# Kernel optimization log

Measured on AMD Instinct MI355X. Metric: run time of the kernel, lower is better.

Reference implementation:

```python
import jax, jax.numpy as jnp
import numpy as np

N_HEAD = 16

def setup_inputs() -> dict:
    key = jax.random.key(0)
    ks = jax.random.split(key, 9)
    B, T, C = 1, 4096, 1024
    s = 1.0 / np.sqrt(C)
    x = jax.random.normal(ks[0], (B, T, C), dtype=jnp.float32)
    Wq = jax.random.uniform(ks[1], (C, C), jnp.float32, -s, s)
    bq = jax.random.uniform(ks[2], (C,), jnp.float32, -s, s)
    Wk = jax.random.uniform(ks[3], (C, C), jnp.float32, -s, s)
    bk = jax.random.uniform(ks[4], (C,), jnp.float32, -s, s)
    Wv = jax.random.uniform(ks[5], (C, C), jnp.float32, -s, s)
    bv = jax.random.uniform(ks[6], (C,), jnp.float32, -s, s)
    Wp = jax.random.uniform(ks[7], (C, C), jnp.float32, -s, s)
    bp = jax.random.uniform(ks[8], (C,), jnp.float32, -s, s)
    return {"x": x, "Wq": Wq, "bq": bq, "Wk": Wk, "bk": bk,
            "Wv": Wv, "bv": bv, "Wp": Wp, "bp": bp}

def reference(x, Wq, bq, Wk, bk, Wv, bv, Wp, bp):
    B, T, C = x.shape
    H = N_HEAD
    D = C // H
    # projections -> (B, H, T, D)
    def proj(W, b):
        return (x @ W.T + b).reshape(B, T, H, D).transpose(0, 2, 1, 3)
    q, k, v = proj(Wq, bq), proj(Wk, bk), proj(Wv, bv)
    scale = 1.0 / np.sqrt(D).astype(np.float32)
    att = jnp.einsum('bhtd,bhsd->bhts', q, k) * scale  # (B,H,T,T)
    causal = jnp.tril(jnp.ones((T, T), dtype=bool))
    att = jnp.where(causal[None, None], att, -jnp.inf)
    att = jax.nn.softmax(att, axis=-1)
    y = jnp.einsum('bhts,bhsd->bhtd', att, v)  # (B,H,T,D)
    y = y.transpose(0, 2, 1, 3).reshape(B, T, C)
    return y @ Wp.T + bp
```

## Files before the change

### kernel.cpp

```cpp
#include <hip/hip_runtime.h>
#include <hip/hip_bf16.h>
#include <math.h>

typedef __bf16 bf16x8 __attribute__((ext_vector_type(8)));
typedef __bf16 bf16x4 __attribute__((ext_vector_type(4)));
typedef float f32x4 __attribute__((ext_vector_type(4)));

#define MFMA_BF16 __builtin_amdgcn_mfma_f32_16x16x32_bf16

#define QSCALE 0.18033688011112042f

__device__ inline void async_load16(const __hip_bfloat16* g, __hip_bfloat16* l) {
    __builtin_amdgcn_global_load_lds(
        (const __attribute__((address_space(1))) unsigned int*)g,
        (__attribute__((address_space(3))) unsigned int*)l,
        16, 0, 0);
}

__device__ inline int sig(int x) {
    return (x & ~12) | ((x & 4) << 1) | ((x & 8) >> 1);
}

__device__ inline unsigned int pack_bf16_trunc(float lo, float hi) {
    return __builtin_amdgcn_perm(__float_as_uint(hi), __float_as_uint(lo),
                                 0x07060302u);
}

__global__ __launch_bounds__(256) void f32_to_bf16(
    const float* __restrict__ in, __hip_bfloat16* __restrict__ out, int n)
{
    const int i = (blockIdx.x * 256 + threadIdx.x) * 8;
    if (i >= n) return;
    const float4 a = *(const float4*)(in + i);
    const float4 b = *(const float4*)(in + i + 4);
    __hip_bfloat16 tmp[8];
    tmp[0] = __float2bfloat16(a.x); tmp[1] = __float2bfloat16(a.y);
    tmp[2] = __float2bfloat16(a.z); tmp[3] = __float2bfloat16(a.w);
    tmp[4] = __float2bfloat16(b.x); tmp[5] = __float2bfloat16(b.y);
    tmp[6] = __float2bfloat16(b.z); tmp[7] = __float2bfloat16(b.w);
    *(bf16x8*)(out + i) = *(const bf16x8*)tmp;
}

__global__ __launch_bounds__(256) void f32_to_bf16_w4(
    const float* __restrict__ w0, const float* __restrict__ w1,
    const float* __restrict__ w2, const float* __restrict__ w3,
    __hip_bfloat16* __restrict__ o0, __hip_bfloat16* __restrict__ o1,
    __hip_bfloat16* __restrict__ o2, __hip_bfloat16* __restrict__ o3, int n)
{
    const int y = blockIdx.y;
    const float* in = y == 0 ? w0 : y == 1 ? w1 : y == 2 ? w2 : w3;
    __hip_bfloat16* out = y == 0 ? o0 : y == 1 ? o1 : y == 2 ? o2 : o3;
    const int i = (blockIdx.x * 256 + threadIdx.x) * 8;
    if (i >= n) return;
    const float4 a = *(const float4*)(in + i);
    const float4 b = *(const float4*)(in + i + 4);
    __hip_bfloat16 tmp[8];
    tmp[0] = __float2bfloat16(a.x); tmp[1] = __float2bfloat16(a.y);
    tmp[2] = __float2bfloat16(a.z); tmp[3] = __float2bfloat16(a.w);
    tmp[4] = __float2bfloat16(b.x); tmp[5] = __float2bfloat16(b.y);
    tmp[6] = __float2bfloat16(b.z); tmp[7] = __float2bfloat16(b.w);
    *(bf16x8*)(out + i) = *(const bf16x8*)tmp;
}

__global__ __launch_bounds__(256) void transpose_bf16(
    const __hip_bfloat16* __restrict__ in, __hip_bfloat16* __restrict__ out,
    int R, int Cc)
{
    __shared__ __align__(16) __hip_bfloat16 tile[64][72];
    const int r0 = blockIdx.x * 64, c0 = blockIdx.y * 64;
    const int tid = threadIdx.x;
    #pragma unroll
    for (int it = 0; it < 2; ++it) {
        const int c = tid + it * 256;
        const int row = c >> 3, col = (c & 7) * 8;
        *(bf16x8*)&tile[row][col] = *(const bf16x8*)(in + (size_t)(r0 + row) * Cc + c0 + col);
    }
    __syncthreads();
    #pragma unroll
    for (int it = 0; it < 2; ++it) {
        const int c = tid + it * 256;
        const int drow = c >> 3, scol = (c & 7) * 8;
        __hip_bfloat16 tmp[8];
        #pragma unroll
        for (int j = 0; j < 8; ++j) tmp[j] = tile[scol + j][drow];
        *(bf16x8*)(out + (size_t)(c0 + drow) * R + r0 + scol) = *(const bf16x8*)tmp;
    }
}

__global__ __launch_bounds__(256) void gemm_qkv(
    const __hip_bfloat16* __restrict__ A,
    const __hip_bfloat16* __restrict__ B,
    const float* __restrict__ bq, const float* __restrict__ bk, const float* __restrict__ bv,
    __hip_bfloat16* __restrict__ Qo, __hip_bfloat16* __restrict__ Ko,
    __hip_bfloat16* __restrict__ Vo,
    int M, int K)
{
    __shared__ __align__(16) __hip_bfloat16 As[128 * 64];
    __shared__ __align__(16) __hip_bfloat16 Bs[128 * 64];

    const int tid  = threadIdx.x;
    const int lane = tid & 63;
    const int wave = tid >> 6;
    const int l15  = lane & 15;
    const int quad = lane >> 4;
    const int m0 = blockIdx.x * 128;
    const int n0 = blockIdx.y * 128;
    const int wr = wave >> 1, wc = wave & 1;
    const int sel = n0 >> 10;

    f32x4 acc[4][4] = {};

    int srow[4], scol[4];
    #pragma unroll
    for (int i = 0; i < 4; ++i) {
        const int c = tid + 256 * i;
        srow[i] = c >> 3;
        scol[i] = ((c & 7) ^ (srow[i] & 7)) * 8;
    }

    for (int k0 = 0; k0 < K; k0 += 64) {
        __syncthreads();
        #pragma unroll
        for (int i = 0; i < 4; ++i) {
            async_load16(A + (size_t)(m0 + srow[i]) * K + k0 + scol[i],
                         As + (size_t)(tid + 256 * i) * 8);
            async_load16(B + (size_t)(n0 + srow[i]) * K + k0 + scol[i],
                         Bs + (size_t)(tid + 256 * i) * 8);
        }
        __syncthreads();

        #pragma unroll
        for (int kd = 0; kd < 2; ++kd) {
            bf16x8 af[4], bfr[4];
            #pragma unroll
            for (int mi = 0; mi < 4; ++mi) {
                const int row = wr * 64 + mi * 16 + l15;
                af[mi] = *(const bf16x8*)(
                    As + row * 64 + (((kd * 4 + quad) ^ (row & 7)) << 3));
            }
            #pragma unroll
            for (int ni = 0; ni < 4; ++ni) {
                const int row = wc * 64 + ni * 16 + l15;
                bfr[ni] = *(const bf16x8*)(
                    Bs + row * 64 + (((kd * 4 + quad) ^ (row & 7)) << 3));
            }
            #pragma unroll
            for (int mi = 0; mi < 4; ++mi)
                #pragma unroll
                for (int ni = 0; ni < 4; ++ni)
                    acc[mi][ni] = MFMA_BF16(af[mi], bfr[ni], acc[mi][ni], 0, 0, 0);
        }
    }

    __hip_bfloat16* dst = sel == 0 ? Qo : (sel == 1 ? Ko : Vo);
    const float* bptr   = sel == 0 ? bq : (sel == 1 ? bk : bv);
    const float sc      = sel == 0 ? QSCALE : 1.0f;

    #pragma unroll
    for (int ni = 0; ni < 4; ++ni) {
        const int cc = (n0 + wc * 64 + ni * 16 + l15) & 1023;
        const float bias = bptr[cc];
        #pragma unroll
        for (int mi = 0; mi < 4; ++mi) {
            const int row = m0 + wr * 64 + mi * 16 + quad * 4;
            #pragma unroll
            for (int r = 0; r < 4; ++r)
                dst[(size_t)(row + r) * 1024 + cc] =
                    __float2bfloat16((acc[mi][ni][r] + bias) * sc);
        }
    }
}

__global__ __launch_bounds__(256) void gemm_out_f32(
    const __hip_bfloat16* __restrict__ A,
    const __hip_bfloat16* __restrict__ B,
    const float* __restrict__ bias,
    float* __restrict__ Cf,
    int M, int N, int K)
{
    __shared__ __align__(16) __hip_bfloat16 As[64 * 64];
    __shared__ __align__(16) __hip_bfloat16 Bs[128 * 64];

    const int tid  = threadIdx.x;
    const int lane = tid & 63;
    const int wave = tid >> 6;
    const int l15  = lane & 15;
    const int quad = lane >> 4;
    const int m0 = blockIdx.x * 64;
    const int n0 = blockIdx.y * 128;
    const int wr = wave >> 1, wc = wave & 1;

    f32x4 acc[2][4] = {};

    int srow[4], scol[4];
    #pragma unroll
    for (int i = 0; i < 4; ++i) {
        const int c = tid + 256 * i;
        srow[i] = c >> 3;
        scol[i] = ((c & 7) ^ (srow[i] & 7)) * 8;
    }

    for (int k0 = 0; k0 < K; k0 += 64) {
        __syncthreads();
        #pragma unroll
        for (int i = 0; i < 2; ++i)
            async_load16(A + (size_t)(m0 + srow[i]) * K + k0 + scol[i],
                         As + (size_t)(tid + 256 * i) * 8);
        #pragma unroll
        for (int i = 0; i < 4; ++i)
            async_load16(B + (size_t)(n0 + srow[i]) * K + k0 + scol[i],
                         Bs + (size_t)(tid + 256 * i) * 8);
        __syncthreads();

        #pragma unroll
        for (int kd = 0; kd < 2; ++kd) {
            bf16x8 af[2], bfr[4];
            #pragma unroll
            for (int mi = 0; mi < 2; ++mi) {
                const int row = wr * 32 + mi * 16 + l15;
                af[mi] = *(const bf16x8*)(
                    As + row * 64 + (((kd * 4 + quad) ^ (row & 7)) << 3));
            }
            #pragma unroll
            for (int ni = 0; ni < 4; ++ni) {
                const int row = wc * 64 + ni * 16 + l15;
                bfr[ni] = *(const bf16x8*)(
                    Bs + row * 64 + (((kd * 4 + quad) ^ (row & 7)) << 3));
            }
            #pragma unroll
            for (int mi = 0; mi < 2; ++mi)
                #pragma unroll
                for (int ni = 0; ni < 4; ++ni)
                    acc[mi][ni] = MFMA_BF16(af[mi], bfr[ni], acc[mi][ni], 0, 0, 0);
        }
    }

    #pragma unroll
    for (int ni = 0; ni < 4; ++ni) {
        const int col = n0 + wc * 64 + ni * 16 + l15;
        const float bv = bias[col];
        #pragma unroll
        for (int mi = 0; mi < 2; ++mi) {
            const int row = m0 + wr * 32 + mi * 16 + quad * 4;
            #pragma unroll
            for (int r = 0; r < 4; ++r)
                Cf[(size_t)(row + r) * N + col] = acc[mi][ni][r] + bv;
        }
    }
}

__global__ __launch_bounds__(512, 4) void attn_causal(
    const __hip_bfloat16* __restrict__ Q,
    const __hip_bfloat16* __restrict__ K,
    const __hip_bfloat16* __restrict__ Vt,
    __hip_bfloat16* __restrict__ PoB,
    float* __restrict__ PlB,
    int T, int C)
{
    const int h  = blockIdx.y;
    const int bx = blockIdx.x;
    const int j  = bx & 7;
    const int sq = bx >> 3;
    const int tid  = threadIdx.x;
    const int w    = tid >> 6;
    const int lane = tid & 63;
    const int l15  = lane & 15;
    const int quad = lane >> 4;

    __hip_bfloat16* Po = PoB + (size_t)sq * T * C;
    float* Pl = PlB + (size_t)sq * (size_t)(T / 64) * 64 * 16;

    const int len1 = j + 1, len2 = 16 - j;
    const int tile1 = j,    tile2 = 15 - j;
    const int kb1 = len1 * sq, kb2 = len2 * sq;

    __shared__ __align__(16) __hip_bfloat16 Ks[2][64 * 64];
    __shared__ __align__(16) __hip_bfloat16 Vts[2][64 * 64];

    const int r0 = tid >> 3, g0 = ((tid & 7) ^ (r0 & 7)) * 8;
    const __hip_bfloat16* Kg0 = K + (size_t)sig(r0) * C + h * 64 + g0;
    const __hip_bfloat16* Vg0 = Vt + (size_t)(h * 64 + r0) * T + g0;

    int koff[2][4], voff[2][4];
    #pragma unroll
    for (int kd = 0; kd < 2; ++kd)
        #pragma unroll
        for (int sb = 0; sb < 4; ++sb) {
            const int kappa = 32 * (sb & 1) + 8 * (l15 >> 2) + 4 * (sb >> 1) + (l15 & 3);
            const int rho = sig(kappa);
            koff[kd][sb] = rho * 64 + (((kd * 4 + quad) ^ (rho & 7)) << 3);
        }
    #pragma unroll
    for (int kk = 0; kk < 2; ++kk)
        #pragma unroll
        for (int db = 0; db < 4; ++db) {
            const int vrow = db * 16 + l15;
            voff[kk][db] = vrow * 64 + (((kk * 4 + quad) ^ (vrow & 7)) << 3);
        }

    bf16x8 ones;
    #pragma unroll
    for (int jj = 0; jj < 8; ++jj) ones[jj] = (__bf16)1.0f;

    int qbase = tile1 * 256 + w * 32;
    bf16x8 aq[2][2];
    #pragma unroll
    for (int rb = 0; rb < 2; ++rb)
        #pragma unroll
        for (int kd = 0; kd < 2; ++kd)
            aq[rb][kd] = *(const bf16x8*)(
                Q + (size_t)(qbase + rb * 16 + l15) * C + h * 64 + kd * 32 + quad * 8);

    f32x4 o[2][4] = {};
    f32x4 lacc[2] = {};

    {
        const size_t so = (size_t)kb1 << 6;
        async_load16(Kg0 + so * C, &Ks[0][tid * 8]);
        async_load16(Vg0 + so, &Vts[0][tid * 8]);
    }

    for (int it = 0; it < 17; ++it) {
        const int kb = (it < len1) ? (kb1 + it) : (kb2 + it - len1);
        const int s0 = kb << 6;
        __syncthreads();
        const int cur = it & 1;
        if (it + 1 < 17) {
            const int kbn = (it + 1 < len1) ? (kb1 + it + 1) : (kb2 + it + 1 - len1);
            const size_t so = (size_t)kbn << 6;
            async_load16(Kg0 + so * C, &Ks[cur ^ 1][tid * 8]);
            async_load16(Vg0 + so, &Vts[cur ^ 1][tid * 8]);
        }

        if (it == len1) {
            #pragma unroll
            for (int rb = 0; rb < 2; ++rb) {
                const int row = qbase + rb * 16 + l15;
                #pragma unroll
                for (int db = 0; db < 4; ++db) {
                    __hip_bfloat16 t[4];
                    #pragma unroll
                    for (int r = 0; r < 4; ++r)
                        t[r] = __float2bfloat16(o[rb][db][r]);
                    *(bf16x4*)(Po + (size_t)row * C + h * 64 + db * 16 + quad * 4)
                        = *(const bf16x4*)t;
                    o[rb][db] = (f32x4){0.f, 0.f, 0.f, 0.f};
                }
                if (quad == 0)
                    Pl[(size_t)h * T + row] = lacc[rb][0];
                lacc[rb] = (f32x4){0.f, 0.f, 0.f, 0.f};
            }
            qbase = tile2 * 256 + w * 32;
            #pragma unroll
            for (int rb = 0; rb < 2; ++rb)
                #pragma unroll
                for (int kd = 0; kd < 2; ++kd)
                    aq[rb][kd] = *(const bf16x8*)(
                        Q + (size_t)(qbase + rb * 16 + l15) * C + h * 64 + kd * 32 + quad * 8);
        }

        if (s0 <= qbase + 31) {
            f32x4 sv[2][4] = {};
            #pragma unroll
            for (int kd = 0; kd < 2; ++kd)
                #pragma unroll
                for (int sb = 0; sb < 4; ++sb) {
                    bf16x8 ak = *(const bf16x8*)(&Ks[cur][koff[kd][sb]]);
                    sv[0][sb] = MFMA_BF16(ak, aq[0][kd], sv[0][sb], 0, 0, 0);
                    sv[1][sb] = MFMA_BF16(ak, aq[1][kd], sv[1][sb], 0, 0, 0);
                }

            const bool diag = (s0 + 63 > qbase);
            bf16x8 bp[2][2];
            #pragma unroll
            for (int rb = 0; rb < 2; ++rb) {
                float pv[4][4];
                #pragma unroll
                for (int sb = 0; sb < 4; ++sb)
                    #pragma unroll
                    for (int r = 0; r < 4; ++r)
                        pv[sb][r] = __builtin_amdgcn_exp2f(sv[rb][sb][r]);
                if (diag) {
                    const int thr = qbase + rb * 16 + l15 - s0 - 8 * quad;
                    #pragma unroll
                    for (int sb = 0; sb < 4; ++sb)
                        #pragma unroll
                        for (int r = 0; r < 4; ++r) {
                            const int c = 32 * (sb & 1) + 4 * (sb >> 1) + r;
                            pv[sb][r] = (c <= thr) ? pv[sb][r] : 0.f;
                        }
                }
                #pragma unroll
                for (int kk = 0; kk < 2; ++kk) {
                    union { unsigned int u[4]; bf16x8 v; } pk;
                    pk.u[0] = pack_bf16_trunc(pv[kk][0], pv[kk][1]);
                    pk.u[1] = pack_bf16_trunc(pv[kk][2], pv[kk][3]);
                    pk.u[2] = pack_bf16_trunc(pv[kk + 2][0], pv[kk + 2][1]);
                    pk.u[3] = pack_bf16_trunc(pv[kk + 2][2], pv[kk + 2][3]);
                    bp[rb][kk] = pk.v;
                }
            }

            lacc[0] = MFMA_BF16(ones, bp[0][0], lacc[0], 0, 0, 0);
            lacc[0] = MFMA_BF16(ones, bp[0][1], lacc[0], 0, 0, 0);
            lacc[1] = MFMA_BF16(ones, bp[1][0], lacc[1], 0, 0, 0);
            lacc[1] = MFMA_BF16(ones, bp[1][1], lacc[1], 0, 0, 0);

            #pragma unroll
            for (int kk = 0; kk < 2; ++kk)
                #pragma unroll
                for (int db = 0; db < 4; ++db) {
                    bf16x8 av = *(const bf16x8*)(&Vts[cur][voff[kk][db]]);
                    o[0][db] = MFMA_BF16(av, bp[0][kk], o[0][db], 0, 0, 0);
                    o[1][db] = MFMA_BF16(av, bp[1][kk], o[1][db], 0, 0, 0);
                }
        }
    }

    #pragma unroll
    for (int rb = 0; rb < 2; ++rb) {
        const int row = qbase + rb * 16 + l15;
        #pragma unroll
        for (int db = 0; db < 4; ++db) {
            __hip_bfloat16 t[4];
            #pragma unroll
            for (int r = 0; r < 4; ++r)
                t[r] = __float2bfloat16(o[rb][db][r]);
            *(bf16x4*)(Po + (size_t)row * C + h * 64 + db * 16 + quad * 4)
                = *(const bf16x4*)t;
        }
        if (quad == 0)
            Pl[(size_t)h * T + row] = lacc[rb][0];
    }
}

__global__ __launch_bounds__(256) void merge_y(
    const __hip_bfloat16* __restrict__ PoB, const float* __restrict__ PlB,
    __hip_bfloat16* __restrict__ Y, int T, int C)
{
    const size_t i = ((size_t)blockIdx.x * 256 + threadIdx.x) * 4;
    const int row = (int)(i / C);
    const int h   = ((int)(i % C)) >> 6;
    const size_t TC = (size_t)T * C;
    const size_t HT = (size_t)T * 16;
    float acc[4] = {0.f, 0.f, 0.f, 0.f};
    float l = 0.f;
    #pragma unroll
    for (int z = 0; z < 4; ++z) {
        bf16x4 a = *(const bf16x4*)(PoB + z * TC + i);
        #pragma unroll
        for (int r = 0; r < 4; ++r)
            acc[r] += __bfloat162float(((const __hip_bfloat16*)&a)[r]);
        l += PlB[z * HT + (size_t)h * T + row];
    }
    const float inv = 1.0f / l;
    __hip_bfloat16 t[4];
    #pragma unroll
    for (int r = 0; r < 4; ++r)
        t[r] = __float2bfloat16(acc[r] * inv);
    *(bf16x4*)(Y + i) = *(const bf16x4*)t;
}

extern "C" void kernel_launch(void* const* d_in, const int* in_sizes, int n_in,
                              void* d_out, int out_size, void* d_ws, size_t ws_size,
                              hipStream_t stream)
{
    const float* x  = (const float*)d_in[0];
    const float* Wq = (const float*)d_in[1];
    const float* bq = (const float*)d_in[2];
    const float* Wk = (const float*)d_in[3];
    const float* bk = (const float*)d_in[4];
    const float* Wv = (const float*)d_in[5];
    const float* bv = (const float*)d_in[6];
    const float* Wp = (const float*)d_in[7];
    const float* bp = (const float*)d_in[8];

    const int C = 1024;
    const int T = in_sizes[0] / C;
    const int H = 16;
    const size_t TC = (size_t)T * C;
    const size_t CC = (size_t)C * C;

    __hip_bfloat16* xb  = (__hip_bfloat16*)d_ws;
    __hip_bfloat16* Wqb = xb + TC;
    __hip_bfloat16* Wkb = Wqb + CC;
    __hip_bfloat16* Wvb = Wkb + CC;
    __hip_bfloat16* Wpb = Wvb + CC;
    __hip_bfloat16* Qw  = Wpb + CC;
    __hip_bfloat16* Kw  = Qw + TC;
    __hip_bfloat16* Vtw = Kw + TC;
    __hip_bfloat16* Vw  = Vtw + TC;
    __hip_bfloat16* PoB = Vw + TC;
    float* PlB = (float*)(PoB + 4 * TC);
    __hip_bfloat16* Yw  = Qw;
    float* out = (float*)d_out;

    f32_to_bf16<<<(int)(TC / 8 / 256), 256, 0, stream>>>(x, xb, (int)TC);
    f32_to_bf16_w4<<<dim3((int)(CC / 8 / 256), 4), 256, 0, stream>>>(
        Wq, Wk, Wv, Wp, Wqb, Wkb, Wvb, Wpb, (int)CC);

    gemm_qkv<<<dim3(T / 128, 3072 / 128), 256, 0, stream>>>(
        xb, Wqb, bq, bk, bv, Qw, Kw, Vw, T, C);

    transpose_bf16<<<dim3(T / 64, C / 64), 256, 0, stream>>>(Vw, Vtw, T, C);

    attn_causal<<<dim3(32, H), 512, 0, stream>>>(
        Qw, Kw, Vtw, PoB, PlB, T, C);

    merge_y<<<(int)(TC / 4 / 256), 256, 0, stream>>>(
        PoB, PlB, Yw, T, C);

    gemm_out_f32<<<dim3(T / 64, C / 128), 256, 0, stream>>>(
        Yw, Wpb, bp, out, T, C, C);
}
```

Baseline: 210.7 us.

## Fuse V transpose into QKV GEMM and split-K merge into attention

Merges the two fp32-to-bf16 conversion launches into one kernel. The V projection tile is now transposed through shared memory inside the QKV GEMM epilogue, which removes the separate transpose kernel and the intermediate V buffer. The merge_y kernel is folded into attention: each block bumps an atomic counter per (tile, head), and the last of four contributors reduces the partial outputs. This cuts several launches and round trips through global memory, at the cost of a memset, atomics, threadfences and extra barriers in the attention kernel.

```diff
diff --git a/kernel.cpp b/kernel.cpp
--- a/kernel.cpp
+++ b/kernel.cpp
@@ -26,65 +26,38 @@
                                  0x07060302u);
 }
 
-__global__ __launch_bounds__(256) void f32_to_bf16(
-    const float* __restrict__ in, __hip_bfloat16* __restrict__ out, int n)
+__global__ __launch_bounds__(256) void convert_all(
+    const float* __restrict__ x,
+    const float* __restrict__ Wq, const float* __restrict__ Wk,
+    const float* __restrict__ Wv, const float* __restrict__ Wp,
+    __hip_bfloat16* __restrict__ xb,
+    __hip_bfloat16* __restrict__ Wqb, __hip_bfloat16* __restrict__ Wkb,
+    __hip_bfloat16* __restrict__ Wvb, __hip_bfloat16* __restrict__ Wpb,
+    int nx, int nw)
 {
-    const int i = (blockIdx.x * 256 + threadIdx.x) * 8;
-    if (i >= n) return;
+    const int xblocks = nx >> 11;
+    const int wblocks = nw >> 11;
+    int b = blockIdx.x;
+    const float* in;
+    __hip_bfloat16* out;
+    int i;
+    if (b < xblocks) {
+        in = x; out = xb; i = (b * 256 + threadIdx.x) * 8;
+    } else {
+        b -= xblocks;
+        const int w = b / wblocks, bb = b - w * wblocks;
+        in  = w == 0 ? Wq : w == 1 ? Wk : w == 2 ? Wv : Wp;
+        out = w == 0 ? Wqb : w == 1 ? Wkb : w == 2 ? Wvb : Wpb;
+        i = (bb * 256 + threadIdx.x) * 8;
+    }
     const float4 a = *(const float4*)(in + i);
-    const float4 b = *(const float4*)(in + i + 4);
+    const float4 c = *(const float4*)(in + i + 4);
     __hip_bfloat16 tmp[8];
     tmp[0] = __float2bfloat16(a.x); tmp[1] = __float2bfloat16(a.y);
     tmp[2] = __float2bfloat16(a.z); tmp[3] = __float2bfloat16(a.w);
-    tmp[4] = __float2bfloat16(b.x); tmp[5] = __float2bfloat16(b.y);
-    tmp[6] = __float2bfloat16(b.z); tmp[7] = __float2bfloat16(b.w);
+    tmp[4] = __float2bfloat16(c.x); tmp[5] = __float2bfloat16(c.y);
+    tmp[6] = __float2bfloat16(c.z); tmp[7] = __float2bfloat16(c.w);
     *(bf16x8*)(out + i) = *(const bf16x8*)tmp;
-}
-
-__global__ __launch_bounds__(256) void f32_to_bf16_w4(
-    const float* __restrict__ w0, const float* __restrict__ w1,
-    const float* __restrict__ w2, const float* __restrict__ w3,
-    __hip_bfloat16* __restrict__ o0, __hip_bfloat16* __restrict__ o1,
-    __hip_bfloat16* __restrict__ o2, __hip_bfloat16* __restrict__ o3, int n)
-{
-    const int y = blockIdx.y;
-    const float* in = y == 0 ? w0 : y == 1 ? w1 : y == 2 ? w2 : w3;
-    __hip_bfloat16* out = y == 0 ? o0 : y == 1 ? o1 : y == 2 ? o2 : o3;
-    const int i = (blockIdx.x * 256 + threadIdx.x) * 8;
-    if (i >= n) return;
-    const float4 a = *(const float4*)(in + i);
-    const float4 b = *(const float4*)(in + i + 4);
-    __hip_bfloat16 tmp[8];
-    tmp[0] = __float2bfloat16(a.x); tmp[1] = __float2bfloat16(a.y);
-    tmp[2] = __float2bfloat16(a.z); tmp[3] = __float2bfloat16(a.w);
-    tmp[4] = __float2bfloat16(b.x); tmp[5] = __float2bfloat16(b.y);
-    tmp[6] = __float2bfloat16(b.z); tmp[7] = __float2bfloat16(b.w);
-    *(bf16x8*)(out + i) = *(const bf16x8*)tmp;
-}
-
-__global__ __launch_bounds__(256) void transpose_bf16(
-    const __hip_bfloat16* __restrict__ in, __hip_bfloat16* __restrict__ out,
-    int R, int Cc)
-{
-    __shared__ __align__(16) __hip_bfloat16 tile[64][72];
-    const int r0 = blockIdx.x * 64, c0 = blockIdx.y * 64;
-    const int tid = threadIdx.x;
-    #pragma unroll
-    for (int it = 0; it < 2; ++it) {
-        const int c = tid + it * 256;
-        const int row = c >> 3, col = (c & 7) * 8;
-        *(bf16x8*)&tile[row][col] = *(const bf16x8*)(in + (size_t)(r0 + row) * Cc + c0 + col);
-    }
-    __syncthreads();
-    #pragma unroll
-    for (int it = 0; it < 2; ++it) {
-        const int c = tid + it * 256;
-        const int drow = c >> 3, scol = (c & 7) * 8;
-        __hip_bfloat16 tmp[8];
-        #pragma unroll
-        for (int j = 0; j < 8; ++j) tmp[j] = tile[scol + j][drow];
-        *(bf16x8*)(out + (size_t)(c0 + drow) * R + r0 + scol) = *(const bf16x8*)tmp;
-    }
 }
 
 __global__ __launch_bounds__(256) void gemm_qkv(
@@ -92,11 +65,12 @@
     const __hip_bfloat16* __restrict__ B,
     const float* __restrict__ bq, const float* __restrict__ bk, const float* __restrict__ bv,
     __hip_bfloat16* __restrict__ Qo, __hip_bfloat16* __restrict__ Ko,
-    __hip_bfloat16* __restrict__ Vo,
+    __hip_bfloat16* __restrict__ Vt,
     int M, int K)
 {
-    __shared__ __align__(16) __hip_bfloat16 As[128 * 64];
-    __shared__ __align__(16) __hip_bfloat16 Bs[128 * 64];
+    __shared__ __align__(16) __hip_bfloat16 smem[2 * 128 * 64];
+    __hip_bfloat16* As = smem;
+    __hip_bfloat16* Bs = smem + 128 * 64;
 
     const int tid  = threadIdx.x;
     const int lane = tid & 63;
@@ -152,21 +126,49 @@
         }
     }
 
-    __hip_bfloat16* dst = sel == 0 ? Qo : (sel == 1 ? Ko : Vo);
-    const float* bptr   = sel == 0 ? bq : (sel == 1 ? bk : bv);
-    const float sc      = sel == 0 ? QSCALE : 1.0f;
-
-    #pragma unroll
-    for (int ni = 0; ni < 4; ++ni) {
-        const int cc = (n0 + wc * 64 + ni * 16 + l15) & 1023;
-        const float bias = bptr[cc];
-        #pragma unroll
-        for (int mi = 0; mi < 4; ++mi) {
-            const int row = m0 + wr * 64 + mi * 16 + quad * 4;
-            #pragma unroll
-            for (int r = 0; r < 4; ++r)
-                dst[(size_t)(row + r) * 1024 + cc] =
-                    __float2bfloat16((acc[mi][ni][r] + bias) * sc);
+    if (sel == 2) {
+        __syncthreads();
+        #pragma unroll
+        for (int ni = 0; ni < 4; ++ni) {
+            const int lc = wc * 64 + ni * 16 + l15;
+            const float bias = bv[(n0 + lc) & 1023];
+            #pragma unroll
+            for (int mi = 0; mi < 4; ++mi) {
+                const int mb = wr * 64 + mi * 16 + quad * 4;
+                const int g = mb >> 3, off = mb & 7;
+                __hip_bfloat16 t[4];
+                #pragma unroll
+                for (int r = 0; r < 4; ++r)
+                    t[r] = __float2bfloat16(acc[mi][ni][r] + bias);
+                *(bf16x4*)(smem + lc * 128 + ((g ^ (lc & 15)) << 3) + off)
+                    = *(const bf16x4*)t;
+            }
+        }
+        __syncthreads();
+        const int cc0 = n0 & 1023;
+        #pragma unroll
+        for (int i = 0; i < 8; ++i) {
+            const int q = tid + 256 * i;
+            const int ch = q >> 4, mg = q & 15;
+            bf16x8 v = *(const bf16x8*)(smem + ch * 128 + ((mg ^ (ch & 15)) << 3));
+            *(bf16x8*)(Vt + (size_t)(cc0 + ch) * M + m0 + mg * 8) = v;
+        }
+    } else {
+        __hip_bfloat16* dst = sel == 0 ? Qo : Ko;
+        const float* bptr   = sel == 0 ? bq : bk;
+        const float sc      = sel == 0 ? QSCALE : 1.0f;
+        #pragma unroll
+        for (int ni = 0; ni < 4; ++ni) {
+            const int cc = (n0 + wc * 64 + ni * 16 + l15) & 1023;
+            const float bias = bptr[cc];
+            #pragma unroll
+            for (int mi = 0; mi < 4; ++mi) {
+                const int row = m0 + wr * 64 + mi * 16 + quad * 4;
+                #pragma unroll
+                for (int r = 0; r < 4; ++r)
+                    dst[(size_t)(row + r) * 1024 + cc] =
+                        __float2bfloat16((acc[mi][ni][r] + bias) * sc);
+            }
         }
     }
 }
@@ -255,6 +257,8 @@
     const __hip_bfloat16* __restrict__ Vt,
     __hip_bfloat16* __restrict__ PoB,
     float* __restrict__ PlB,
+    int* __restrict__ cnt,
+    __hip_bfloat16* __restrict__ Y,
     int T, int C)
 {
     const int h  = blockIdx.y;
@@ -267,8 +271,10 @@
     const int l15  = lane & 15;
     const int quad = lane >> 4;
 
-    __hip_bfloat16* Po = PoB + (size_t)sq * T * C;
-    float* Pl = PlB + (size_t)sq * (size_t)(T / 64) * 64 * 16;
+    const size_t TCs = (size_t)T * C;
+    const size_t HT  = (size_t)T * 16;
+    __hip_bfloat16* Po = PoB + (size_t)sq * TCs;
+    float* Pl = PlB + (size_t)sq * HT;
 
     const int len1 = j + 1, len2 = 16 - j;
     const int tile1 = j,    tile2 = 15 - j;
@@ -276,6 +282,7 @@
 
     __shared__ __align__(16) __hip_bfloat16 Ks[2][64 * 64];
     __shared__ __align__(16) __hip_bfloat16 Vts[2][64 * 64];
+    __shared__ int wonFlags[2];
 
     const int r0 = tid >> 3, g0 = ((tid & 7) ^ (r0 & 7)) * 8;
     const __hip_bfloat16* Kg0 = K + (size_t)sig(r0) * C + h * 64 + g0;
@@ -350,6 +357,10 @@
                     Pl[(size_t)h * T + row] = lacc[rb][0];
                 lacc[rb] = (f32x4){0.f, 0.f, 0.f, 0.f};
             }
+            __threadfence();
+            __syncthreads();
+            if (tid == 0)
+                wonFlags[0] = (atomicAdd(&cnt[tile1 * 16 + h], 1) == 3);
             qbase = tile2 * 256 + w * 32;
             #pragma unroll
             for (int rb = 0; rb < 2; ++rb)
@@ -432,33 +443,43 @@
         if (quad == 0)
             Pl[(size_t)h * T + row] = lacc[rb][0];
     }
-}
-
-__global__ __launch_bounds__(256) void merge_y(
-    const __hip_bfloat16* __restrict__ PoB, const float* __restrict__ PlB,
-    __hip_bfloat16* __restrict__ Y, int T, int C)
-{
-    const size_t i = ((size_t)blockIdx.x * 256 + threadIdx.x) * 4;
-    const int row = (int)(i / C);
-    const int h   = ((int)(i % C)) >> 6;
-    const size_t TC = (size_t)T * C;
-    const size_t HT = (size_t)T * 16;
-    float acc[4] = {0.f, 0.f, 0.f, 0.f};
-    float l = 0.f;
-    #pragma unroll
-    for (int z = 0; z < 4; ++z) {
-        bf16x4 a = *(const bf16x4*)(PoB + z * TC + i);
-        #pragma unroll
-        for (int r = 0; r < 4; ++r)
-            acc[r] += __bfloat162float(((const __hip_bfloat16*)&a)[r]);
-        l += PlB[z * HT + (size_t)h * T + row];
-    }
-    const float inv = 1.0f / l;
-    __hip_bfloat16 t[4];
-    #pragma unroll
-    for (int r = 0; r < 4; ++r)
-        t[r] = __float2bfloat16(acc[r] * inv);
-    *(bf16x4*)(Y + i) = *(const bf16x4*)t;
+    __threadfence();
+    __syncthreads();
+    if (tid == 0)
+        wonFlags[1] = (atomicAdd(&cnt[tile2 * 16 + h], 1) == 3);
+    __syncthreads();
+
+    #pragma unroll
+    for (int e = 0; e < 2; ++e) {
+        const int tl = e == 0 ? tile1 : tile2;
+        if (wonFlags[e]) {
+            __threadfence();
+            #pragma unroll
+            for (int i = 0; i < 4; ++i) {
+                const int qc = tid + 512 * i;
+                const int r  = qc >> 3;
+                const int c8 = (qc & 7) * 8;
+                const int row = tl * 256 + r;
+                const size_t base = (size_t)row * C + h * 64 + c8;
+                float a8[8] = {};
+                float l = 0.f;
+                #pragma unroll
+                for (int z = 0; z < 4; ++z) {
+                    bf16x8 a = *(const bf16x8*)(PoB + (size_t)z * TCs + base);
+                    #pragma unroll
+                    for (int rr = 0; rr < 8; ++rr)
+                        a8[rr] += (float)(((const __bf16*)&a)[rr]);
+                    l += PlB[(size_t)z * HT + (size_t)h * T + row];
+                }
+                const float inv = 1.0f / l;
+                __hip_bfloat16 t[8];
+                #pragma unroll
+                for (int rr = 0; rr < 8; ++rr)
+                    t[rr] = __float2bfloat16(a8[rr] * inv);
+                *(bf16x8*)(Y + base) = *(const bf16x8*)t;
+            }
+        }
+    }
 }
 
 extern "C" void kernel_launch(void* const* d_in, const int* in_sizes, int n_in,
@@ -489,26 +510,22 @@
     __hip_bfloat16* Qw  = Wpb + CC;
     __hip_bfloat16* Kw  = Qw + TC;
     __hip_bfloat16* Vtw = Kw + TC;
-    __hip_bfloat16* Vw  = Vtw + TC;
-    __hip_bfloat16* PoB = Vw + TC;
+    __hip_bfloat16* PoB = Vtw + TC;
     float* PlB = (float*)(PoB + 4 * TC);
+    int* cnt = (int*)(PlB + 4 * (size_t)T * 16);
     __hip_bfloat16* Yw  = Qw;
     float* out = (float*)d_out;
 
-    f32_to_bf16<<<(int)(TC / 8 / 256), 256, 0, stream>>>(x, xb, (int)TC);
-    f32_to_bf16_w4<<<dim3((int)(CC / 8 / 256), 4), 256, 0, stream>>>(
-        Wq, Wk, Wv, Wp, Wqb, Wkb, Wvb, Wpb, (int)CC);
+    convert_all<<<(int)(TC / 2048 + 4 * CC / 2048), 256, 0, stream>>>(
+        x, Wq, Wk, Wv, Wp, xb, Wqb, Wkb, Wvb, Wpb, (int)TC, (int)CC);
 
     gemm_qkv<<<dim3(T / 128, 3072 / 128), 256, 0, stream>>>(
-        xb, Wqb, bq, bk, bv, Qw, Kw, Vw, T, C);
-
-    transpose_bf16<<<dim3(T / 64, C / 64), 256, 0, stream>>>(Vw, Vtw, T, C);
+        xb, Wqb, bq, bk, bv, Qw, Kw, Vtw, T, C);
+
+    hipMemsetAsync(cnt, 0, 16 * 16 * sizeof(int), stream);
 
     attn_causal<<<dim3(32, H), 512, 0, stream>>>(
-        Qw, Kw, Vtw, PoB, PlB, T, C);
-
-    merge_y<<<(int)(TC / 4 / 256), 256, 0, stream>>>(
-        PoB, PlB, Yw, T, C);
+        Qw, Kw, Vtw, PoB, PlB, cnt, Yw, T, C);
 
     gemm_out_f32<<<dim3(T / 64, C / 128), 256, 0, stream>>>(
         Yw, Wpb, bp, out, T, C, C);
```

Result: slower. 548.7 us (+160.5%).
